# Performance work log

Measured on AMD Instinct MI355X. Metric: run time of the kernel, lower is better.

Reference implementation:

```python
import jax, jax.numpy as jnp
import numpy as np
import math

HIDDEN = 256
NUM_HEADS = 8
HEAD_DIM = HIDDEN // NUM_HEADS  # 32
SCALE = math.sqrt(HEAD_DIM)
B, N, E = 1, 20000, 320000


def setup_inputs() -> dict:
    key = jax.random.key(0)
    kq, kk, kv, ke = jax.random.split(key, 4)
    q = jax.random.normal(kq, (B, N, HIDDEN), dtype=jnp.float32)
    k = jax.random.normal(kk, (B, N, HIDDEN), dtype=jnp.float32)
    v = jax.random.normal(kv, (B, N, HIDDEN), dtype=jnp.float32)
    edge_index = jax.random.randint(ke, (2, E), 0, N, dtype=jnp.int64)
    return {"q": q, "k": k, "v": v, "edge_index": edge_index}


def reference(q, k, v, edge_index):
    batch_size, node_num = q.shape[0], q.shape[1]
    # flatten batch*node axis, split heads: [B*N, H, D]
    qf = q.reshape(-1, NUM_HEADS, HEAD_DIM)
    kf = k.reshape(-1, NUM_HEADS, HEAD_DIM)
    vf = v.reshape(-1, NUM_HEADS, HEAD_DIM)
    src_idx = edge_index[0]
    dst_idx = edge_index[1]
    src = kf[src_idx]    # [E, H, D] gathered keys
    dest = qf[dst_idx]   # [E, H, D] gathered queries
    # unnormalized exp score per edge/head, clamped like the torch code
    score = jnp.clip(jnp.sum(src * dest, axis=-1, keepdims=True) / SCALE, -5.0, 5.0)
    score = jnp.exp(score)                 # [E, H, 1]
    msg = vf[src_idx] * score              # [E, H, D]
    num_seg = qf.shape[0]
    wV = jax.ops.segment_sum(msg, dst_idx, num_segments=num_seg)    # [B*N, H, D]
    Z = jax.ops.segment_sum(score, dst_idx, num_segments=num_seg)   # [B*N, H, 1]
    x = wV / (Z + 1e-6)
    return x.reshape(batch_size, node_num, -1)
```

## Files before the change

kernel.cpp:

```cpp
#include <hip/hip_runtime.h>
#include <hip/hip_fp16.h>
#include <math.h>

#define NHEADS 8
#define HIDDEN 256
#define F4_PER_ROW 64
#define INV_SCALE 0.17677669529663687f
#define ELL_W 64

#define SCAN_THREADS 1024
#define SCAN_CHUNK 20


union H4 { float2 f; __half2 h[2]; };
union KV8 { float4 f4; __half2 h2[4]; };

__global__ void __launch_bounds__(256)
build_kernel(const float4* __restrict__ kf4, const float4* __restrict__ vf4,
             char* __restrict__ kv,
             const int* __restrict__ src, const int* __restrict__ dst,
             int* __restrict__ cnt, int* __restrict__ ell,
             int nf4, int E) {
    int stride = gridDim.x * blockDim.x;
    int tid0 = blockIdx.x * blockDim.x + threadIdx.x;

    for (int i = tid0; i < nf4; i += stride) {
        int n = i >> 6;
        int c = i & 63;
        char* base = kv + (size_t)n * 1024 + (size_t)c * 8;
        float4 x = kf4[i];
        H4 u;
        u.h[0] = __floats2half2_rn(x.x, x.y);
        u.h[1] = __floats2half2_rn(x.z, x.w);
        *(float2*)base = u.f;
        float4 y = vf4[i];
        H4 w;
        w.h[0] = __floats2half2_rn(y.x, y.y);
        w.h[1] = __floats2half2_rn(y.z, y.w);
        *(float2*)(base + 512) = w.f;
    }

    int nq = E >> 2;
    for (int q = tid0; q < nq; q += stride) {
        int4 s = ((const int4*)src)[q];
        int4 d = ((const int4*)dst)[q];
        int sl;
        sl = atomicAdd(&cnt[d.x], 1); if (sl < ELL_W) ell[d.x * ELL_W + sl] = s.x;
        sl = atomicAdd(&cnt[d.y], 1); if (sl < ELL_W) ell[d.y * ELL_W + sl] = s.y;
        sl = atomicAdd(&cnt[d.z], 1); if (sl < ELL_W) ell[d.z * ELL_W + sl] = s.z;
        sl = atomicAdd(&cnt[d.w], 1); if (sl < ELL_W) ell[d.w * ELL_W + sl] = s.w;
    }
    if (tid0 == 0) {
        for (int i = (E >> 2) << 2; i < E; ++i) {
            int t = dst[i];
            int sl = atomicAdd(&cnt[t], 1);
            if (sl < ELL_W) ell[t * ELL_W + sl] = src[i];
        }
    }
}

__device__ __forceinline__ float edge_score(const KV8& u, float4 qa, float4 qb) {
    float2 p0 = __half22float2(u.h2[0]);
    float2 p1 = __half22float2(u.h2[1]);
    float2 p2 = __half22float2(u.h2[2]);
    float2 p3 = __half22float2(u.h2[3]);
    float r = p0.x * qa.x + p0.y * qa.y + p1.x * qa.z + p1.y * qa.w
            + p2.x * qb.x + p2.y * qb.y + p3.x * qb.z + p3.y * qb.w;
    r += __shfl_xor(r, 1, 4);
    r += __shfl_xor(r, 2, 4);
    return __expf(fminf(fmaxf(r * INV_SCALE, -5.f), 5.f));
}

__device__ __forceinline__ void acc8(const KV8& u, float sc, float* acc) {
    float2 w0 = __half22float2(u.h2[0]);
    float2 w1 = __half22float2(u.h2[1]);
    float2 w2 = __half22float2(u.h2[2]);
    float2 w3 = __half22float2(u.h2[3]);
    acc[0] += w0.x * sc; acc[1] += w0.y * sc;
    acc[2] += w1.x * sc; acc[3] += w1.y * sc;
    acc[4] += w2.x * sc; acc[5] += w2.y * sc;
    acc[6] += w3.x * sc; acc[7] += w3.y * sc;
}

__global__ void __launch_bounds__(256)
gather16_kernel(const float4* __restrict__ q4, const char* __restrict__ kv,
                const int* __restrict__ cnt, const int* __restrict__ ell,
                float4* __restrict__ out4, int N) {
    int wid  = threadIdx.x >> 6;
    int lane = threadIdx.x & 63;
    int t = blockIdx.x * 4 + wid;
    if (t >= N) return;

    int deg = cnt[t];
    deg = deg < ELL_W ? deg : ELL_W;
    const int* lst = ell + (size_t)t * ELL_W;

    long trow = (long)t * F4_PER_ROW;
    int lk = lane & 31;
    float4 qa = q4[trow + 2 * lk];
    float4 qb = q4[trow + 2 * lk + 1];
    int srcLane = lk & ~3;

    float acc[8] = {0.f, 0.f, 0.f, 0.f, 0.f, 0.f, 0.f, 0.f};
    float z = 0.f;
    size_t lo = (size_t)lane * 16;

    int i = 0;
    for (; i + 4 <= deg; i += 4) {
        int4 ss = *(const int4*)(lst + i);
        KV8 u0, u1, u2, u3;
        u0.f4 = *(const float4*)(kv + (size_t)ss.x * 1024 + lo);
        u1.f4 = *(const float4*)(kv + (size_t)ss.y * 1024 + lo);
        u2.f4 = *(const float4*)(kv + (size_t)ss.z * 1024 + lo);
        u3.f4 = *(const float4*)(kv + (size_t)ss.w * 1024 + lo);

        float s0 = edge_score(u0, qa, qb);
        float s1 = edge_score(u1, qa, qb);
        float s2 = edge_score(u2, qa, qb);
        float s3 = edge_score(u3, qa, qb);
        z += s0 + s1 + s2 + s3;

        float b0 = __shfl(s0, srcLane, 64);
        float b1 = __shfl(s1, srcLane, 64);
        float b2 = __shfl(s2, srcLane, 64);
        float b3 = __shfl(s3, srcLane, 64);

        acc8(u0, b0, acc);
        acc8(u1, b1, acc);
        acc8(u2, b2, acc);
        acc8(u3, b3, acc);
    }
    for (; i < deg; ++i) {
        int s = lst[i];
        KV8 u;
        u.f4 = *(const float4*)(kv + (size_t)s * 1024 + lo);
        float sc = edge_score(u, qa, qb);
        z += sc;
        float b = __shfl(sc, srcLane, 64);
        acc8(u, b, acc);
    }

    float zf = __shfl(z, srcLane, 64);
    float inv = 1.f / (zf + 1e-6f);
    if (lane >= 32) {
        int j = lane - 32;
        float4 o1 = make_float4(acc[0] * inv, acc[1] * inv, acc[2] * inv, acc[3] * inv);
        float4 o2 = make_float4(acc[4] * inv, acc[5] * inv, acc[6] * inv, acc[7] * inv);
        out4[trow + 2 * j]     = o1;
        out4[trow + 2 * j + 1] = o2;
    }
}


__global__ void __launch_bounds__(256)
histogram_kernel(const int* __restrict__ dst, int* __restrict__ cnt, int E) {
    int i = (blockIdx.x * blockDim.x + threadIdx.x) * 4;
    if (i + 3 < E) {
        int4 d = *(const int4*)(dst + i);
        atomicAdd(&cnt[d.x], 1);
        atomicAdd(&cnt[d.y], 1);
        atomicAdd(&cnt[d.z], 1);
        atomicAdd(&cnt[d.w], 1);
    } else {
        for (; i < E; ++i) atomicAdd(&cnt[dst[i]], 1);
    }
}

__global__ void __launch_bounds__(SCAN_THREADS)
scan_kernel(const int* __restrict__ cnt, int* __restrict__ off, int N) {
    __shared__ int wsum[16];
    __shared__ int wpre[16];
    int t = threadIdx.x;
    int lane = t & 63;
    int wv = t >> 6;
    int base = t * SCAN_CHUNK;
    int local[SCAN_CHUNK];
    int sum = 0;
    #pragma unroll
    for (int j = 0; j < SCAN_CHUNK; ++j) {
        int i = base + j;
        int c = (i < N) ? cnt[i] : 0;
        local[j] = c;
        sum += c;
    }
    int x = sum;
    #pragma unroll
    for (int d = 1; d < 64; d <<= 1) {
        int y = __shfl_up(x, d, 64);
        if (lane >= d) x += y;
    }
    if (lane == 63) wsum[wv] = x;
    __syncthreads();
    if (t < 16) {
        int v = wsum[t];
        #pragma unroll
        for (int d = 1; d < 16; d <<= 1) {
            int y = __shfl_up(v, d, 16);
            if (t >= d) v += y;
        }
        wpre[t] = v;
    }
    __syncthreads();
    int run = (wv ? wpre[wv - 1] : 0) + (x - sum);
    #pragma unroll
    for (int j = 0; j < SCAN_CHUNK; ++j) {
        int i = base + j;
        if (i <= N) off[i] = run;
        run += local[j];
    }
}

__global__ void __launch_bounds__(256)
scatter_kernel(const int* __restrict__ src, const int* __restrict__ dst,
               const int* __restrict__ off, int* __restrict__ cnt,
               int* __restrict__ csr_src, int E) {
    int i = (blockIdx.x * blockDim.x + threadIdx.x) * 4;
    if (i + 3 < E) {
        int4 s = *(const int4*)(src + i);
        int4 d = *(const int4*)(dst + i);
        csr_src[off[d.x] + atomicSub(&cnt[d.x], 1) - 1] = s.x;
        csr_src[off[d.y] + atomicSub(&cnt[d.y], 1) - 1] = s.y;
        csr_src[off[d.z] + atomicSub(&cnt[d.z], 1) - 1] = s.z;
        csr_src[off[d.w] + atomicSub(&cnt[d.w], 1) - 1] = s.w;
    } else {
        for (; i < E; ++i) {
            int t = dst[i];
            csr_src[off[t] + atomicSub(&cnt[t], 1) - 1] = src[i];
        }
    }
}

__device__ __forceinline__ float dot4(float4 a, float4 b) {
    return a.x * b.x + a.y * b.y + a.z * b.z + a.w * b.w;
}

__device__ __forceinline__ float hred8(float p) {
    #pragma unroll
    for (int m = 1; m < 8; m <<= 1) p += __shfl_xor(p, m, 8);
    return p;
}

__global__ void __launch_bounds__(256)
gather_kernel(const float4* __restrict__ q4, const float4* __restrict__ k4,
              const float4* __restrict__ v4, const int* __restrict__ csr_src,
              const int* __restrict__ off, float4* __restrict__ out4, int N) {
    int wid  = threadIdx.x >> 6;
    int lane = threadIdx.x & 63;
    int t = blockIdx.x * 4 + wid;
    if (t >= N) return;

    int beg = off[t], end = off[t + 1];
    long trow = (long)t * F4_PER_ROW;
    float4 qv = q4[trow + lane];

    float4 acc = make_float4(0.f, 0.f, 0.f, 0.f);
    float z = 0.f;

    for (int i = beg; i < end; ++i) {
        int s = csr_src[i];
        long r = (long)s * F4_PER_ROW + lane;
        float4 kv = k4[r];
        float4 vv = v4[r];
        float p = hred8(dot4(kv, qv));
        float sc = __expf(fminf(fmaxf(p * INV_SCALE, -5.f), 5.f));
        acc.x += vv.x * sc;
        acc.y += vv.y * sc;
        acc.z += vv.z * sc;
        acc.w += vv.w * sc;
        z += sc;
    }

    float inv = 1.f / (z + 1e-6f);
    float4 o;
    o.x = acc.x * inv; o.y = acc.y * inv; o.z = acc.z * inv; o.w = acc.w * inv;
    out4[trow + lane] = o;
}


extern "C" void kernel_launch(void* const* d_in, const int* in_sizes, int n_in,
                              void* d_out, int out_size, void* d_ws, size_t ws_size,
                              hipStream_t stream) {
    const float* qf = (const float*)d_in[0];
    const float* kf = (const float*)d_in[1];
    const float* vf = (const float*)d_in[2];
    const int*   ei = (const int*)d_in[3];

    int E = in_sizes[3] / 2;
    int N = in_sizes[0] / HIDDEN;
    int nf4 = in_sizes[0] / 4;

    const int* src = ei;
    const int* dst = ei + E;

    size_t need = (size_t)N * 1024 + (size_t)N * ELL_W * 4 + (size_t)N * 4 + 256;

    if (ws_size >= need) {
        char* p = (char*)d_ws;
        char* kv  = p;                       p += (size_t)N * 1024;
        int*  ell = (int*)p;                 p += (size_t)N * ELL_W * 4;
        int*  cnt = (int*)p;

        hipMemsetAsync(cnt, 0, (size_t)N * sizeof(int), stream);
        build_kernel<<<4096, 256, 0, stream>>>(
            (const float4*)kf, (const float4*)vf, kv,
            src, dst, cnt, ell, nf4, E);
        gather16_kernel<<<(N + 3) / 4, 256, 0, stream>>>(
            (const float4*)qf, kv, cnt, ell, (float4*)d_out, N);
    } else {
        int* cnt = (int*)d_ws;
        int* off = cnt + N;
        int* csr = off + N + 1;

        hipMemsetAsync(cnt, 0, (size_t)N * sizeof(int), stream);
        int eb = (E / 4 + 255) / 256 + 1;
        histogram_kernel<<<eb, 256, 0, stream>>>(dst, cnt, E);
        scan_kernel<<<1, SCAN_THREADS, 0, stream>>>(cnt, off, N);
        scatter_kernel<<<eb, 256, 0, stream>>>(src, dst, off, cnt, csr, E);
        gather_kernel<<<(N + 3) / 4, 256, 0, stream>>>(
            (const float4*)qf, (const float4*)kf, (const float4*)vf,
            csr, off, (float4*)d_out, N);
    }
}
```

Before: 160.2 us.

## Double-buffer neighbor KV loads in batches of eight in gather kernel

Replaces the unroll-by-4 neighbor loop with a software pipeline. Batches of 8 gathered fp16 K/V rows are prefetched into one register buffer while the previous batch is scored and accumulated. Tail edges are padded by clamping the index and masking the score to zero, and a zero-degree early exit writes zeros. This aims to hide gather latency by keeping more loads in flight, at the cost of more registers (two 8-entry float4 buffers), lower occupancy, and wasted loads on padded tail slots (average degree is about 16).

Result: slower. 180.1 us (+12.4%).

```diff
diff --git a/kernel.cpp b/kernel.cpp
--- a/kernel.cpp
+++ b/kernel.cpp
@@ -7,6 +7,7 @@
 #define F4_PER_ROW 64
 #define INV_SCALE 0.17677669529663687f
 #define ELL_W 64
+#define UB 8
 
 #define SCAN_THREADS 1024
 #define SCAN_CHUNK 20
@@ -82,6 +83,31 @@
     acc[6] += w3.x * sc; acc[7] += w3.y * sc;
 }
 
+__device__ __forceinline__ void issue_batch(const char* __restrict__ kv,
+                                            const int* __restrict__ lst,
+                                            int deg, int base, size_t lo, KV8* u) {
+    #pragma unroll
+    for (int j = 0; j < UB; ++j) {
+        int pos = base + j;
+        int ij = pos < deg ? pos : deg - 1;
+        int s = lst[ij];
+        u[j].f4 = *(const float4*)(kv + (size_t)s * 1024 + lo);
+    }
+}
+
+__device__ __forceinline__ void consume_batch(const KV8* u, int deg, int base,
+                                              float4 qa, float4 qb, int srcLane,
+                                              float* acc, float& z) {
+    #pragma unroll
+    for (int j = 0; j < UB; ++j) {
+        float sc = edge_score(u[j], qa, qb);
+        sc = (base + j < deg) ? sc : 0.f;
+        z += sc;
+        float b = __shfl(sc, srcLane, 64);
+        acc8(u[j], b, acc);
+    }
+}
+
 __global__ void __launch_bounds__(256)
 gather16_kernel(const float4* __restrict__ q4, const char* __restrict__ kv,
                 const int* __restrict__ cnt, const int* __restrict__ ell,
@@ -97,6 +123,17 @@
 
     long trow = (long)t * F4_PER_ROW;
     int lk = lane & 31;
+
+    if (deg == 0) {
+        if (lane >= 32) {
+            int j = lane - 32;
+            float4 zr = make_float4(0.f, 0.f, 0.f, 0.f);
+            out4[trow + 2 * j]     = zr;
+            out4[trow + 2 * j + 1] = zr;
+        }
+        return;
+    }
+
     float4 qa = q4[trow + 2 * lk];
     float4 qb = q4[trow + 2 * lk + 1];
     int srcLane = lk & ~3;
@@ -105,39 +142,23 @@
     float z = 0.f;
     size_t lo = (size_t)lane * 16;
 
-    int i = 0;
-    for (; i + 4 <= deg; i += 4) {
-        int4 ss = *(const int4*)(lst + i);
-        KV8 u0, u1, u2, u3;
-        u0.f4 = *(const float4*)(kv + (size_t)ss.x * 1024 + lo);
-        u1.f4 = *(const float4*)(kv + (size_t)ss.y * 1024 + lo);
-        u2.f4 = *(const float4*)(kv + (size_t)ss.z * 1024 + lo);
-        u3.f4 = *(const float4*)(kv + (size_t)ss.w * 1024 + lo);
-
-        float s0 = edge_score(u0, qa, qb);
-        float s1 = edge_score(u1, qa, qb);
-        float s2 = edge_score(u2, qa, qb);
-        float s3 = edge_score(u3, qa, qb);
-        z += s0 + s1 + s2 + s3;
-
-        float b0 = __shfl(s0, srcLane, 64);
-        float b1 = __shfl(s1, srcLane, 64);
-        float b2 = __shfl(s2, srcLane, 64);
-        float b3 = __shfl(s3, srcLane, 64);
-
-        acc8(u0, b0, acc);
-        acc8(u1, b1, acc);
-        acc8(u2, b2, acc);
-        acc8(u3, b3, acc);
-    }
-    for (; i < deg; ++i) {
-        int s = lst[i];
-        KV8 u;
-        u.f4 = *(const float4*)(kv + (size_t)s * 1024 + lo);
-        float sc = edge_score(u, qa, qb);
-        z += sc;
-        float b = __shfl(sc, srcLane, 64);
-        acc8(u, b, acc);
+    KV8 A[UB], B[UB];
+    issue_batch(kv, lst, deg, 0, lo, A);
+    int nb = (deg + UB - 1) / UB;
+
+    int bi = 1;
+    for (; bi + 1 < nb; bi += 2) {
+        issue_batch(kv, lst, deg, bi * UB, lo, B);
+        consume_batch(A, deg, (bi - 1) * UB, qa, qb, srcLane, acc, z);
+        issue_batch(kv, lst, deg, (bi + 1) * UB, lo, A);
+        consume_batch(B, deg, bi * UB, qa, qb, srcLane, acc, z);
+    }
+    if (bi < nb) {
+        issue_batch(kv, lst, deg, bi * UB, lo, B);
+        consume_batch(A, deg, (bi - 1) * UB, qa, qb, srcLane, acc, z);
+        consume_batch(B, deg, bi * UB, qa, qb, srcLane, acc, z);
+    } else {
+        consume_batch(A, deg, (bi - 1) * UB, qa, qb, srcLane, acc, z);
     }
 
     float zf = __shfl(z, srcLane, 64);
```

## Split KV staging buffer per head and gather one head per wavefront

Applied to the files above, without the earlier changes.

The fp16 K/V staging buffer changes from one 1 KB row per node to a per-head layout of 128-byte rows (K and V interleaved for each head). The gather kernel now gives each wavefront one (node, head) pair, with 8 lanes per edge and 8 edges processed in parallel. Edge indices are held in a register and broadcast with shuffles, and partial sums are combined across edge groups with xor-shuffle reductions at the end. The aim is to use more parallelism on low-degree nodes and keep each head's gathered data in a compact region. The cost is 8x more wavefronts, repeated loads of cnt/ell and q per head, and extra reduction shuffles.

Result: slower. 184.1 us (+14.9%).

```diff
diff --git a/kernel.cpp b/kernel.cpp
--- a/kernel.cpp
+++ b/kernel.cpp
@@ -17,27 +17,29 @@
 
 __global__ void __launch_bounds__(256)
 build_kernel(const float4* __restrict__ kf4, const float4* __restrict__ vf4,
-             char* __restrict__ kv,
+             char* __restrict__ kvh,
              const int* __restrict__ src, const int* __restrict__ dst,
              int* __restrict__ cnt, int* __restrict__ ell,
-             int nf4, int E) {
+             int nf4, int N, int E) {
     int stride = gridDim.x * blockDim.x;
     int tid0 = blockIdx.x * blockDim.x + threadIdx.x;
 
     for (int i = tid0; i < nf4; i += stride) {
         int n = i >> 6;
         int c = i & 63;
-        char* base = kv + (size_t)n * 1024 + (size_t)c * 8;
+        int hk = c >> 3;
+        int off = (c & 7) * 8;
+        char* bb = kvh + ((size_t)hk * N + n) * 128 + off;
         float4 x = kf4[i];
         H4 u;
         u.h[0] = __floats2half2_rn(x.x, x.y);
         u.h[1] = __floats2half2_rn(x.z, x.w);
-        *(float2*)base = u.f;
+        *(float2*)bb = u.f;
         float4 y = vf4[i];
         H4 w;
         w.h[0] = __floats2half2_rn(y.x, y.y);
         w.h[1] = __floats2half2_rn(y.z, y.w);
-        *(float2*)(base + 512) = w.f;
+        *(float2*)(bb + 64) = w.f;
     }
 
     int nq = E >> 2;
@@ -59,95 +61,88 @@
     }
 }
 
-__device__ __forceinline__ float edge_score(const KV8& u, float4 qa, float4 qb) {
-    float2 p0 = __half22float2(u.h2[0]);
-    float2 p1 = __half22float2(u.h2[1]);
-    float2 p2 = __half22float2(u.h2[2]);
-    float2 p3 = __half22float2(u.h2[3]);
-    float r = p0.x * qa.x + p0.y * qa.y + p1.x * qa.z + p1.y * qa.w
-            + p2.x * qb.x + p2.y * qb.y + p3.x * qb.z + p3.y * qb.w;
-    r += __shfl_xor(r, 1, 4);
-    r += __shfl_xor(r, 2, 4);
-    return __expf(fminf(fmaxf(r * INV_SCALE, -5.f), 5.f));
-}
-
-__device__ __forceinline__ void acc8(const KV8& u, float sc, float* acc) {
-    float2 w0 = __half22float2(u.h2[0]);
-    float2 w1 = __half22float2(u.h2[1]);
-    float2 w2 = __half22float2(u.h2[2]);
-    float2 w3 = __half22float2(u.h2[3]);
-    acc[0] += w0.x * sc; acc[1] += w0.y * sc;
-    acc[2] += w1.x * sc; acc[3] += w1.y * sc;
-    acc[4] += w2.x * sc; acc[5] += w2.y * sc;
-    acc[6] += w3.x * sc; acc[7] += w3.y * sc;
-}
-
-__global__ void __launch_bounds__(256)
-gather16_kernel(const float4* __restrict__ q4, const char* __restrict__ kv,
-                const int* __restrict__ cnt, const int* __restrict__ ell,
-                float4* __restrict__ out4, int N) {
-    int wid  = threadIdx.x >> 6;
+__global__ void __launch_bounds__(256)
+gather_hs_kernel(const float* __restrict__ qf, const char* __restrict__ kvh,
+                 const int* __restrict__ cnt, const int* __restrict__ ell,
+                 float* __restrict__ outf, int N) {
+    int b = blockIdx.x;
+    int h = b & 7;
+    int wid = threadIdx.x >> 6;
     int lane = threadIdx.x & 63;
-    int t = blockIdx.x * 4 + wid;
+    int t = (b >> 3) * 4 + wid;
     if (t >= N) return;
+
+    int sub = lane & 7;
+    int eg  = lane >> 3;
+
+    const float* qsl = qf + (size_t)t * HIDDEN + h * 32;
+    float* ob = outf + (size_t)t * HIDDEN + h * 32;
 
     int deg = cnt[t];
     deg = deg < ELL_W ? deg : ELL_W;
+
+    if (deg == 0) {
+        if (eg == 0 && sub >= 4) {
+            float4 zr = make_float4(0.f, 0.f, 0.f, 0.f);
+            ((float4*)ob)[(sub - 4) * 2]     = zr;
+            ((float4*)ob)[(sub - 4) * 2 + 1] = zr;
+        }
+        return;
+    }
+
     const int* lst = ell + (size_t)t * ELL_W;
-
-    long trow = (long)t * F4_PER_ROW;
-    int lk = lane & 31;
-    float4 qa = q4[trow + 2 * lk];
-    float4 qb = q4[trow + 2 * lk + 1];
-    int srcLane = lk & ~3;
+    int idxreg = 0;
+    if (lane < deg) idxreg = lst[lane];
+
+    int qsub = sub & 3;
+    float4 qa = ((const float4*)qsl)[qsub * 2];
+    float4 qb = ((const float4*)qsl)[qsub * 2 + 1];
+
+    const char* base = kvh + (size_t)h * N * 128;
 
     float acc[8] = {0.f, 0.f, 0.f, 0.f, 0.f, 0.f, 0.f, 0.f};
     float z = 0.f;
-    size_t lo = (size_t)lane * 16;
-
-    int i = 0;
-    for (; i + 4 <= deg; i += 4) {
-        int4 ss = *(const int4*)(lst + i);
-        KV8 u0, u1, u2, u3;
-        u0.f4 = *(const float4*)(kv + (size_t)ss.x * 1024 + lo);
-        u1.f4 = *(const float4*)(kv + (size_t)ss.y * 1024 + lo);
-        u2.f4 = *(const float4*)(kv + (size_t)ss.z * 1024 + lo);
-        u3.f4 = *(const float4*)(kv + (size_t)ss.w * 1024 + lo);
-
-        float s0 = edge_score(u0, qa, qb);
-        float s1 = edge_score(u1, qa, qb);
-        float s2 = edge_score(u2, qa, qb);
-        float s3 = edge_score(u3, qa, qb);
-        z += s0 + s1 + s2 + s3;
-
-        float b0 = __shfl(s0, srcLane, 64);
-        float b1 = __shfl(s1, srcLane, 64);
-        float b2 = __shfl(s2, srcLane, 64);
-        float b3 = __shfl(s3, srcLane, 64);
-
-        acc8(u0, b0, acc);
-        acc8(u1, b1, acc);
-        acc8(u2, b2, acc);
-        acc8(u3, b3, acc);
-    }
-    for (; i < deg; ++i) {
-        int s = lst[i];
+
+    int nb = (deg + 7) >> 3;
+    for (int it = 0; it < nb; ++it) {
+        int p = it * 8 + eg;
+        int pc = p < deg ? p : deg - 1;
+        int s = __shfl(idxreg, pc, 64);
         KV8 u;
-        u.f4 = *(const float4*)(kv + (size_t)s * 1024 + lo);
-        float sc = edge_score(u, qa, qb);
+        u.f4 = *(const float4*)(base + (size_t)s * 128 + sub * 16);
+
+        float2 a0 = __half22float2(u.h2[0]);
+        float2 a1 = __half22float2(u.h2[1]);
+        float2 a2 = __half22float2(u.h2[2]);
+        float2 a3 = __half22float2(u.h2[3]);
+        float r = a0.x * qa.x + a0.y * qa.y + a1.x * qa.z + a1.y * qa.w
+                + a2.x * qb.x + a2.y * qb.y + a3.x * qb.z + a3.y * qb.w;
+        r += __shfl_xor(r, 1, 8);
+        r += __shfl_xor(r, 2, 8);
+        float sc = __expf(fminf(fmaxf(r * INV_SCALE, -5.f), 5.f));
+        sc = __shfl(sc, lane & ~7, 64);
+        sc = (p < deg) ? sc : 0.f;
         z += sc;
-        float b = __shfl(sc, srcLane, 64);
-        acc8(u, b, acc);
-    }
-
-    float zf = __shfl(z, srcLane, 64);
-    float inv = 1.f / (zf + 1e-6f);
-    if (lane >= 32) {
-        int j = lane - 32;
+        acc[0] += a0.x * sc; acc[1] += a0.y * sc;
+        acc[2] += a1.x * sc; acc[3] += a1.y * sc;
+        acc[4] += a2.x * sc; acc[5] += a2.y * sc;
+        acc[6] += a3.x * sc; acc[7] += a3.y * sc;
+    }
+
+    #pragma unroll
+    for (int m = 8; m < 64; m <<= 1) {
+        z += __shfl_xor(z, m, 64);
+        #pragma unroll
+        for (int d = 0; d < 8; ++d) acc[d] += __shfl_xor(acc[d], m, 64);
+    }
+
+    float inv = 1.f / (z + 1e-6f);
+    if (eg == 0 && sub >= 4) {
+        int j = sub - 4;
         float4 o1 = make_float4(acc[0] * inv, acc[1] * inv, acc[2] * inv, acc[3] * inv);
         float4 o2 = make_float4(acc[4] * inv, acc[5] * inv, acc[6] * inv, acc[7] * inv);
-        out4[trow + 2 * j]     = o1;
-        out4[trow + 2 * j + 1] = o2;
+        ((float4*)ob)[j * 2]     = o1;
+        ((float4*)ob)[j * 2 + 1] = o2;
     }
 }
 
@@ -296,16 +291,17 @@
 
     if (ws_size >= need) {
         char* p = (char*)d_ws;
-        char* kv  = p;                       p += (size_t)N * 1024;
+        char* kvh = p;                       p += (size_t)N * 1024;
         int*  ell = (int*)p;                 p += (size_t)N * ELL_W * 4;
         int*  cnt = (int*)p;
 
         hipMemsetAsync(cnt, 0, (size_t)N * sizeof(int), stream);
         build_kernel<<<4096, 256, 0, stream>>>(
-            (const float4*)kf, (const float4*)vf, kv,
-            src, dst, cnt, ell, nf4, E);
-        gather16_kernel<<<(N + 3) / 4, 256, 0, stream>>>(
-            (const float4*)qf, kv, cnt, ell, (float4*)d_out, N);
+            (const float4*)kf, (const float4*)vf, kvh,
+            src, dst, cnt, ell, nf4, N, E);
+        int ngrp = (N + 3) / 4;
+        gather_hs_kernel<<<8 * ngrp, 256, 0, stream>>>(
+            qf, kvh, cnt, ell, (float*)d_out, N);
     } else {
         int* cnt = (int*)d_ws;
         int* off = cnt + N;
```
